# Kernel optimization log

Hardware: AMD Instinct MI355X
Metric: run time of the kernel (lower is better)

Reference implementation:

```python
import jax, jax.numpy as jnp
import numpy as np

R, K, D = 4096, 128, 128      # num_records, num_codes, code_dim
B, P = 8, 8192                # batch_size, num_points
DIST_SCALE = 2.0
IN_DIM = D + 3                # 131


def setup_inputs() -> dict:
    key = jax.random.key(0)
    ks = jax.random.split(key, 20)
    inp = {}
    inp["indices"] = jax.random.randint(ks[0], (B,), 0, R)
    inp["query_points"] = jax.random.uniform(ks[1], (B, P, 3)) - 0.5
    inp["codes_position"] = jax.random.uniform(ks[2], (R, K, 3)) - 0.5
    inp["codes"] = jax.random.normal(ks[3], (R, K, D)) * 0.01
    dims = [(IN_DIM, 2048), (IN_DIM + 2048, 1024), (IN_DIM + 1024, 512),
            (IN_DIM + 512, 256), (IN_DIM + 256, 128), (128, 1)]
    for i, (fi, fo) in enumerate(dims):
        inp[f"W{i+1}"] = jax.random.normal(ks[4 + 2 * i], (fi, fo)) * (1.0 / np.sqrt(fi))
        inp[f"b{i+1}"] = jnp.zeros((fo,), jnp.float32)
    return inp


def _lrelu(x):
    return jnp.where(x > 0, x, 0.02 * x)


def reference(indices, query_points, codes_position, codes,
              W1, b1, W2, b2, W3, b3, W4, b4, W5, b5, W6, b6):
    # CodeCloud.query
    bcp = codes_position[indices]                      # (B,K,3)
    bc = codes[indices]                                # (B,K,D)
    diff = query_points[:, :, None, :] - bcp[:, None, :, :]   # (B,P,K,3)
    square_dist = jnp.sum(diff * diff, axis=-1) + 1e-16       # (B,P,K)
    # 1/sqrt(sd)**s == sd**(-s/2)
    weight = square_dist ** (-DIST_SCALE / 2.0)
    weight = weight / jnp.sum(weight, axis=-1, keepdims=True)
    query_codes = jnp.einsum('bpk,bkd->bpd', weight, bc)      # (B,P,D)

    # IM_Decoder with skip concats
    x = jnp.concatenate([query_codes, query_points], axis=-1) # (B,P,IN_DIM)
    h = _lrelu(x @ W1 + b1); h = jnp.concatenate([h, x], axis=-1)
    h = _lrelu(h @ W2 + b2); h = jnp.concatenate([h, x], axis=-1)
    h = _lrelu(h @ W3 + b3); h = jnp.concatenate([h, x], axis=-1)
    h = _lrelu(h @ W4 + b4); h = jnp.concatenate([h, x], axis=-1)
    h = _lrelu(h @ W5 + b5)
    pred_sd = (h @ W6 + b6)[..., 0]                            # (B,P)
    return pred_sd
```

## Files before the change

kernel.cpp:

```cpp
#include <hip/hip_runtime.h>
#include <cstdint>
#include <cstddef>

typedef unsigned short u16;
typedef __attribute__((ext_vector_type(8))) short short8;
typedef __attribute__((ext_vector_type(8))) unsigned short us8;
typedef __attribute__((ext_vector_type(4))) unsigned short us4;
typedef __attribute__((ext_vector_type(4))) float f32x4;

#define BATCH 8
#define PTS   8192
#define NPTS  (BATCH * PTS)
#define KC    128
#define DC    128

__device__ __forceinline__ float bf2f(u16 h) {
  union { unsigned u; float f; } v; v.u = ((unsigned)h) << 16; return v.f;
}
__device__ __forceinline__ u16 f2bf(float f) {
  union { float f; unsigned u; } v; v.f = f;
  unsigned r = v.u + 0x7FFFu + ((v.u >> 16) & 1u);
  return (u16)(r >> 16);
}

__device__ __forceinline__ bool detect_f32(const u16* p, int lane) {
  float v = bf2f(p[2 * lane]);
  float av = v < 0.f ? -v : v;
  return __ballot(av > 4.0f) != 0ULL;
}

__device__ __forceinline__ float ldf(const void* p, size_t i, bool f32) {
  return f32 ? ((const float*)p)[i] : bf2f(((const u16*)p)[i]);
}

__device__ __forceinline__ void gload16(const void* g, void* l) {
  __builtin_amdgcn_global_load_lds(
      (const __attribute__((address_space(1))) unsigned int*)(uintptr_t)g,
      (__attribute__((address_space(3))) unsigned int*)(uintptr_t)l,
      16, 0, 0);
}

__global__ __launch_bounds__(256)
void transpose_w(const void* __restrict__ W, u16* __restrict__ Wt,
                 int fi, int fo, int kp) {
  const bool f32 = detect_f32((const u16*)W, threadIdx.x & 63);
  __shared__ __align__(16) u16 tile[32][33];
  const int k0 = blockIdx.x * 32;
  const int n0 = blockIdx.y * 32;
  const int tx = threadIdx.x & 31;
  const int ty = threadIdx.x >> 5;
  #pragma unroll
  for (int i = 0; i < 4; ++i) {
    int k = k0 + ty + 8 * i;
    u16 v = 0;
    if (k < fi) {
      size_t idx = (size_t)k * fo + (n0 + tx);
      v = f32 ? f2bf(((const float*)W)[idx]) : ((const u16*)W)[idx];
    }
    tile[ty + 8 * i][tx] = v;
  }
  __syncthreads();
  #pragma unroll
  for (int i = 0; i < 4; ++i) {
    int n = n0 + ty + 8 * i;
    Wt[(size_t)n * kp + (k0 + tx)] = tile[tx][ty + 8 * i];
  }
}

__global__ __launch_bounds__(256)
void interp_kernel(const int* __restrict__ indices,
                   const void* __restrict__ qp,
                   const void* __restrict__ cp,
                   const void* __restrict__ codes,
                   u16* __restrict__ d0, int ld0,
                   u16* __restrict__ d1, int ld1,
                   u16* __restrict__ d2, int ld2,
                   u16* __restrict__ d3, int ld3,
                   u16* __restrict__ d4, int ld4,
                   int m0) {
  __shared__ __align__(16) u16 s_bc[KC * DC];
  __shared__ float s_cp[KC * 3];
  __shared__ float s_qp[32 * 3];
  __shared__ float s_w[32 * 132];
  __shared__ float s_part[32 * 4];
  __shared__ float s_winv[32];

  const int t = threadIdx.x;
  const bool f32 = detect_f32((const u16*)codes, t & 63);
  const int row0 = blockIdx.x * 32;
  const int gp0 = m0 + row0;
  const int b = gp0 / PTS;
  const int rec = indices[b];

  if (f32) {
    const float* src = (const float*)codes + (size_t)rec * (KC * DC);
    #pragma unroll
    for (int i = 0; i < 16; ++i) {
      int off = (t + i * 256) * 4;
      float4 v = *(const float4*)&src[off];
      us4 o; o.x = f2bf(v.x); o.y = f2bf(v.y); o.z = f2bf(v.z); o.w = f2bf(v.w);
      *(us4*)&s_bc[off] = o;
    }
  } else {
    const u16* src = (const u16*)codes + (size_t)rec * (KC * DC);
    #pragma unroll
    for (int i = 0; i < 8; ++i) {
      int off = (t + i * 256) * 8;
      *(us8*)&s_bc[off] = *(const us8*)&src[off];
    }
  }
  if (t < KC) {
    size_t base = ((size_t)rec * KC + t) * 3;
    s_cp[t * 3 + 0] = ldf(cp, base + 0, f32);
    s_cp[t * 3 + 1] = ldf(cp, base + 1, f32);
    s_cp[t * 3 + 2] = ldf(cp, base + 2, f32);
  }
  if (t < 96) {
    int i = t / 3, c = t - i * 3;
    s_qp[t] = ldf(qp, (size_t)(gp0 + i) * 3 + c, f32);
  }
  __syncthreads();

  #pragma unroll
  for (int it = 0; it < 16; ++it) {
    int idx = t + it * 256;
    int k = idx & 127, p = idx >> 7;
    float dx = s_qp[p * 3 + 0] - s_cp[k * 3 + 0];
    float dy = s_qp[p * 3 + 1] - s_cp[k * 3 + 1];
    float dz = s_qp[p * 3 + 2] - s_cp[k * 3 + 2];
    float dsq = dx * dx + dy * dy + dz * dz + 1e-16f;
    s_w[p * 132 + k] = 1.0f / dsq;
  }
  __syncthreads();
  if (t < 128) {
    int p = t >> 2, part = t & 3;
    float s = 0.f;
    #pragma unroll
    for (int j = 0; j < 32; ++j) s += s_w[p * 132 + part * 32 + j];
    s_part[p * 4 + part] = s;
  }
  __syncthreads();
  if (t < 32) {
    float s = s_part[t * 4 + 0] + s_part[t * 4 + 1] + s_part[t * 4 + 2] + s_part[t * 4 + 3];
    s_winv[t] = 1.0f / s;
  }
  __syncthreads();

  {
    int p = t >> 3;
    int dd = (t & 7) * 16;
    float acc[16];
    #pragma unroll
    for (int j = 0; j < 16; ++j) acc[j] = 0.f;
    for (int k = 0; k < KC; ++k) {
      float wv = s_w[p * 132 + k];
      us8 v0 = *(const us8*)&s_bc[k * DC + dd];
      us8 v1 = *(const us8*)&s_bc[k * DC + dd + 8];
      #pragma unroll
      for (int j = 0; j < 8; ++j) acc[j] += wv * bf2f(v0[j]);
      #pragma unroll
      for (int j = 0; j < 8; ++j) acc[8 + j] += wv * bf2f(v1[j]);
    }
    float wi = s_winv[p];
    us8 o0, o1;
    #pragma unroll
    for (int j = 0; j < 8; ++j) { o0[j] = f2bf(acc[j] * wi); o1[j] = f2bf(acc[8 + j] * wi); }
    size_t row = (size_t)(row0 + p);
    *(us8*)&d0[row * ld0 + dd] = o0; *(us8*)&d0[row * ld0 + dd + 8] = o1;
    *(us8*)&d1[row * ld1 + dd] = o0; *(us8*)&d1[row * ld1 + dd + 8] = o1;
    *(us8*)&d2[row * ld2 + dd] = o0; *(us8*)&d2[row * ld2 + dd + 8] = o1;
    *(us8*)&d3[row * ld3 + dd] = o0; *(us8*)&d3[row * ld3 + dd + 8] = o1;
    *(us8*)&d4[row * ld4 + dd] = o0; *(us8*)&d4[row * ld4 + dd + 8] = o1;
  }

  if (t < 32) {
    size_t row = (size_t)(row0 + t);
    us8 z = {0, 0, 0, 0, 0, 0, 0, 0};
    us8 t0 = z;
    t0[0] = f2bf(s_qp[t * 3 + 0]);
    t0[1] = f2bf(s_qp[t * 3 + 1]);
    t0[2] = f2bf(s_qp[t * 3 + 2]);
    u16* ps[5] = {d0, d1, d2, d3, d4};
    int  ls[5] = {ld0, ld1, ld2, ld3, ld4};
    #pragma unroll
    for (int qd = 0; qd < 5; ++qd) {
      u16* dst = ps[qd] + row * ls[qd] + 128;
      *(us8*)&dst[0] = t0;
      #pragma unroll
      for (int c = 1; c < 8; ++c) *(us8*)&dst[c * 8] = z;
    }
  }
}

__global__ __launch_bounds__(256, 2)
void gemm_bt_lrelu(const u16* __restrict__ A, int lda,
                   const u16* __restrict__ Bt, int ldb,
                   const u16* __restrict__ bias,
                   u16* __restrict__ C, int ldc,
                   int Kp) {
  __shared__ __align__(16) u16 sA[128 * 32];
  __shared__ __align__(16) u16 sB[128 * 32];
  const int tid = threadIdx.x;
  const int lane = tid & 63;
  const int w = tid >> 6;
  const int wm = w & 1, wn = w >> 1;
  const int bn = blockIdx.x * 128, bm = blockIdx.y * 128;

  const f32x4 zero = {0.f, 0.f, 0.f, 0.f};
  f32x4 acc[4][4];
  #pragma unroll
  for (int i = 0; i < 4; ++i)
    #pragma unroll
    for (int j = 0; j < 4; ++j) acc[i][j] = zero;

  const int r4 = lane >> 2;
  const int cg = lane & 3;
  const u16* ag = A + (size_t)(bm + w * 32 + r4) * lda + cg * 8;
  const u16* bg = Bt + (size_t)(bn + w * 32 + r4) * ldb + cg * 8;
  u16* la = &sA[w * 1024];
  u16* lb = &sB[w * 1024];

  const int r = lane & 15, q = lane >> 4;
  const u16* ra = &sA[(wm * 64 + r) * 32 + q * 8];
  const u16* rb = &sB[(wn * 64 + r) * 32 + q * 8];

  for (int k0 = 0; k0 < Kp; k0 += 32) {
    gload16(ag + k0, la);
    gload16(ag + k0 + (size_t)16 * lda, la + 512);
    gload16(bg + k0, lb);
    gload16(bg + k0 + (size_t)16 * ldb, lb + 512);
    __syncthreads();
    short8 af[4], bq[4];
    #pragma unroll
    for (int mt = 0; mt < 4; ++mt) af[mt] = *(const short8*)(ra + mt * 512);
    #pragma unroll
    for (int nt = 0; nt < 4; ++nt) bq[nt] = *(const short8*)(rb + nt * 512);
    #pragma unroll
    for (int mt = 0; mt < 4; ++mt)
      #pragma unroll
      for (int nt = 0; nt < 4; ++nt)
        acc[mt][nt] = __builtin_amdgcn_mfma_f32_16x16x32_bf16(af[mt], bq[nt], acc[mt][nt], 0, 0, 0);
    __syncthreads();
  }

  #pragma unroll
  for (int nt = 0; nt < 4; ++nt) {
    int col = bn + wn * 64 + nt * 16 + r;
    float bb = bf2f(bias[col]);
    #pragma unroll
    for (int mt = 0; mt < 4; ++mt) {
      int grow = bm + wm * 64 + mt * 16 + q * 4;
      #pragma unroll
      for (int reg = 0; reg < 4; ++reg) {
        float v = acc[mt][nt][reg] + bb;
        v = v > 0.f ? v : 0.02f * v;
        C[(size_t)(grow + reg) * ldc + col] = f2bf(v);
      }
    }
  }
}

#define G_BAR()  __builtin_amdgcn_s_barrier()
#define G_FENCE() asm volatile("" ::: "memory")
#define G_LGKM0() asm volatile("s_waitcnt lgkmcnt(0)" ::: "memory")

__global__ __launch_bounds__(512, 2)
void gemm256_bt_lrelu(const u16* __restrict__ A, int lda,
                      const u16* __restrict__ Bt, int ldb,
                      const u16* __restrict__ bias,
                      u16* __restrict__ C, int ldc,
                      int Kp, int lognx) {
  __shared__ __align__(16) u16 sA[32768];
  __shared__ __align__(16) u16 sB[32768];

  const int tid = threadIdx.x;
  const int lane = tid & 63;
  const int w = tid >> 6;
  const int wm = w >> 2;
  const int wn = w & 3;
  const int lr = lane & 15;
  const int kg = lane >> 4;
  const int rs = tid >> 3;
  const int cs = ((tid & 7) ^ (rs & 7)) << 3;

  const unsigned nwg = gridDim.x;
  const unsigned lid = blockIdx.x;
  const unsigned qq = nwg >> 3, rr = nwg & 7, xc = lid & 7, ii = lid >> 3;
  const unsigned swz = (xc < rr ? xc * (qq + 1) : rr * (qq + 1) + (xc - rr) * qq) + ii;
  const int bx = (int)(swz & ((1u << lognx) - 1u));
  const int by = (int)(swz >> lognx);
  const int bn = bx << 8, bm = by << 8;

  const u16* a0 = A + (size_t)(bm + rs) * lda + cs;
  const u16* b0 = Bt + (size_t)(bn + rs) * ldb + cs;

  const int rowA = (wm << 13) + (lr << 6);
  const int rowB = (wn << 12) + (lr << 6);
  const int c0 = ((kg ^ (lr & 7)) << 3);
  const int c1 = (((4 + kg) ^ (lr & 7)) << 3);

  const int nt = Kp >> 6;

  f32x4 acc[8][4];
  const f32x4 zero = {0.f, 0.f, 0.f, 0.f};
  #pragma unroll
  for (int m = 0; m < 8; ++m)
    #pragma unroll
    for (int n = 0; n < 4; ++n) acc[m][n] = zero;

#define STAGE_A(bfv, h, kt) do { \
    const u16* _s = a0 + (size_t)(h) * 128 * lda + ((kt) << 6); \
    u16* _d = &sA[((bfv) << 14) + ((h) << 13) + (tid << 3)]; \
    gload16(_s, _d); \
    gload16(_s + (size_t)64 * lda, _d + 4096); \
  } while (0)
#define STAGE_B(bfv, h, kt) do { \
    const u16* _s = b0 + (size_t)(h) * 128 * ldb + ((kt) << 6); \
    u16* _d = &sB[((bfv) << 14) + ((h) << 13) + (tid << 3)]; \
    gload16(_s, _d); \
    gload16(_s + (size_t)64 * ldb, _d + 4096); \
  } while (0)

  STAGE_B(0, 0, 0); STAGE_B(0, 1, 0); STAGE_A(0, 0, 0); STAGE_A(0, 1, 0);
  if (nt > 1) {
    STAGE_B(1, 0, 1); STAGE_B(1, 1, 1); STAGE_A(1, 0, 1);
    asm volatile("s_waitcnt vmcnt(6)" ::: "memory");
  } else {
    asm volatile("s_waitcnt vmcnt(0)" ::: "memory");
  }
  G_BAR(); G_FENCE();

  short8 af[4][2], bq[4][2];

  for (int t = 0; t < nt; ++t) {
    const int sb = (t & 1) << 14;
    #pragma unroll
    for (int m = 0; m < 4; ++m) {
      af[m][0] = *(const short8*)&sA[sb + rowA + (m << 10) + c0];
      af[m][1] = *(const short8*)&sA[sb + rowA + (m << 10) + c1];
    }
    #pragma unroll
    for (int n = 0; n < 4; ++n) {
      bq[n][0] = *(const short8*)&sB[sb + rowB + (n << 10) + c0];
      bq[n][1] = *(const short8*)&sB[sb + rowB + (n << 10) + c1];
    }
    if (t + 1 < nt) STAGE_A((t & 1) ^ 1, 1, t + 1);
    G_FENCE(); G_BAR(); G_FENCE();
    __builtin_amdgcn_s_setprio(1);
    #pragma unroll
    for (int k = 0; k < 2; ++k)
      #pragma unroll
      for (int m = 0; m < 4; ++m)
        #pragma unroll
        for (int n = 0; n < 2; ++n)
          acc[m][n] = __builtin_amdgcn_mfma_f32_16x16x32_bf16(af[m][k], bq[n][k], acc[m][n], 0, 0, 0);
    __builtin_amdgcn_s_setprio(0);
    G_LGKM0();
    G_BAR(); G_FENCE();
    if (t + 2 < nt) STAGE_B(t & 1, 0, t + 2);
    G_FENCE(); G_BAR(); G_FENCE();
    __builtin_amdgcn_s_setprio(1);
    #pragma unroll
    for (int k = 0; k < 2; ++k)
      #pragma unroll
      for (int m = 0; m < 4; ++m)
        #pragma unroll
        for (int n = 0; n < 2; ++n)
          acc[m][n + 2] = __builtin_amdgcn_mfma_f32_16x16x32_bf16(af[m][k], bq[n + 2][k], acc[m][n + 2], 0, 0, 0);
    __builtin_amdgcn_s_setprio(0);
    G_BAR(); G_FENCE();
    #pragma unroll
    for (int m = 0; m < 4; ++m) {
      af[m][0] = *(const short8*)&sA[sb + rowA + ((m + 4) << 10) + c0];
      af[m][1] = *(const short8*)&sA[sb + rowA + ((m + 4) << 10) + c1];
    }
    if (t + 2 < nt) STAGE_B(t & 1, 1, t + 2);
    G_FENCE(); G_BAR(); G_FENCE();
    __builtin_amdgcn_s_setprio(1);
    #pragma unroll
    for (int k = 0; k < 2; ++k)
      #pragma unroll
      for (int m = 0; m < 4; ++m)
        #pragma unroll
        for (int n = 0; n < 2; ++n)
          acc[m + 4][n] = __builtin_amdgcn_mfma_f32_16x16x32_bf16(af[m][k], bq[n][k], acc[m + 4][n], 0, 0, 0);
    __builtin_amdgcn_s_setprio(0);
    G_LGKM0();
    G_BAR(); G_FENCE();
    if (t + 2 < nt) STAGE_A(t & 1, 0, t + 2);
    G_FENCE(); G_BAR(); G_FENCE();
    __builtin_amdgcn_s_setprio(1);
    #pragma unroll
    for (int k = 0; k < 2; ++k)
      #pragma unroll
      for (int m = 0; m < 4; ++m)
        #pragma unroll
        for (int n = 0; n < 2; ++n)
          acc[m + 4][n + 2] = __builtin_amdgcn_mfma_f32_16x16x32_bf16(af[m][k], bq[n + 2][k], acc[m + 4][n + 2], 0, 0, 0);
    __builtin_amdgcn_s_setprio(0);
    if (t + 2 < nt)      { asm volatile("s_waitcnt vmcnt(6)" ::: "memory"); }
    else if (t + 1 < nt) { asm volatile("s_waitcnt vmcnt(0)" ::: "memory"); }
    G_BAR(); G_FENCE();
  }
#undef STAGE_A
#undef STAGE_B

  const int colb = bn + (wn << 6);
  const int rowb = bm + (wm << 7);
  #pragma unroll
  for (int n = 0; n < 4; ++n) {
    const int col = colb + n * 16 + lr;
    const float bb = bf2f(bias[col]);
    #pragma unroll
    for (int m = 0; m < 8; ++m) {
      const int grow = rowb + m * 16 + kg * 4;
      #pragma unroll
      for (int reg = 0; reg < 4; ++reg) {
        float v = acc[m][n][reg] + bb;
        v = v > 0.f ? v : 0.02f * v;
        C[(size_t)(grow + reg) * ldc + col] = f2bf(v);
      }
    }
  }
}

__global__ __launch_bounds__(256)
void final_dot(const u16* __restrict__ h5, const void* __restrict__ W6,
               const u16* __restrict__ b6, void* __restrict__ out, int m0) {
  __shared__ float s_w6[128];
  const int t = threadIdx.x;
  const bool f32 = detect_f32((const u16*)W6, t & 63);
  if (t < 128) s_w6[t] = ldf(W6, t, f32);
  __syncthreads();
  const size_t row = (size_t)blockIdx.x * 256 + t;
  const u16* hp = h5 + row * 128;
  float acc = 0.f;
  #pragma unroll
  for (int i = 0; i < 16; ++i) {
    us8 v = *(const us8*)&hp[i * 8];
    #pragma unroll
    for (int j = 0; j < 8; ++j) acc += bf2f(v[j]) * s_w6[i * 8 + j];
  }
  acc += bf2f(b6[0]);
  if (f32) ((float*)out)[m0 + row] = acc;
  else     ((u16*)out)[m0 + row] = f2bf(acc);
}

extern "C" void kernel_launch(void* const* d_in, const int* in_sizes, int n_in,
                              void* d_out, int out_size, void* d_ws, size_t ws_size,
                              hipStream_t stream) {
  (void)in_sizes; (void)n_in; (void)out_size;
  const int* indices = (const int*)d_in[0];
  const void* qp    = d_in[1];
  const void* cp    = d_in[2];
  const void* codes = d_in[3];
  const void* Wm[6]; const u16* bv[6];
  for (int i = 0; i < 6; ++i) { Wm[i] = d_in[4 + 2 * i]; bv[i] = (const u16*)d_in[5 + 2 * i]; }

  static const int fi[5] = {131, 2179, 1155, 643, 387};
  static const int fo[5] = {2048, 1024, 512, 256, 128};
  static const int kp[5] = {192, 2240, 1216, 704, 448};
  static const int bw[6] = {192, 2240, 1216, 704, 448, 128};

  char* base = (char*)d_ws;
  size_t off = 0;
  u16* wt[5];
  for (int l = 0; l < 5; ++l) {
    wt[l] = (u16*)(base + off);
    off = (off + (size_t)kp[l] * fo[l] * 2 + 255) & ~(size_t)255;
  }
  const size_t fixed = off;

  int CH = 128;
  for (int c = 1; c <= 128; c <<= 1) {
    size_t mc = (size_t)NPTS / c;
    size_t need = fixed;
    for (int i = 0; i < 6; ++i) need += ((mc * bw[i] * 2 + 255) & ~(size_t)255);
    if (need <= ws_size) { CH = c; break; }
  }
  const size_t Mc = (size_t)NPTS / CH;
  u16* ab[6];
  for (int i = 0; i < 6; ++i) {
    ab[i] = (u16*)(base + off);
    off = (off + Mc * bw[i] * 2 + 255) & ~(size_t)255;
  }

  for (int l = 0; l < 5; ++l) {
    dim3 g(kp[l] / 32, fo[l] / 32);
    hipLaunchKernelGGL(transpose_w, g, dim3(256), 0, stream, Wm[l], wt[l], fi[l], fo[l], kp[l]);
  }

  const int nM256 = (int)(Mc >> 8);
  const int nM128 = (int)(Mc >> 7);
  for (int c = 0; c < CH; ++c) {
    int m0 = (int)((size_t)c * Mc);
    hipLaunchKernelGGL(interp_kernel, dim3((unsigned)(Mc / 32)), dim3(256), 0, stream,
                       indices, qp, cp, codes,
                       ab[0], 192,
                       ab[1] + 2048, 2240,
                       ab[2] + 1024, 1216,
                       ab[3] + 512, 704,
                       ab[4] + 256, 448,
                       m0);
    hipLaunchKernelGGL(gemm256_bt_lrelu, dim3((unsigned)(8 * nM256)), dim3(512), 0, stream,
                       ab[0], 192,  wt[0], 192,  bv[0], ab[1], 2240, 192,  3);
    hipLaunchKernelGGL(gemm256_bt_lrelu, dim3((unsigned)(4 * nM256)), dim3(512), 0, stream,
                       ab[1], 2240, wt[1], 2240, bv[1], ab[2], 1216, 2240, 2);
    hipLaunchKernelGGL(gemm256_bt_lrelu, dim3((unsigned)(2 * nM256)), dim3(512), 0, stream,
                       ab[2], 1216, wt[2], 1216, bv[2], ab[3], 704,  1216, 1);
    hipLaunchKernelGGL(gemm256_bt_lrelu, dim3((unsigned)(1 * nM256)), dim3(512), 0, stream,
                       ab[3], 704,  wt[3], 704,  bv[3], ab[4], 448,  704,  0);
    hipLaunchKernelGGL(gemm_bt_lrelu, dim3(1, (unsigned)nM128), dim3(256), 0, stream,
                       ab[4], 448,  wt[4], 448,  bv[4], ab[5], 128,  448);
    hipLaunchKernelGGL(final_dot, dim3((unsigned)(Mc / 256)), dim3(256), 0, stream,
                       ab[5], Wm[5], bv[5], (void*)d_out, m0);
  }
}
```

Baseline: 1.021 ms.

## Stage GEMM epilogue through LDS for coalesced 16-byte output stores

Swaps the MFMA operand order so each lane holds four consecutive output columns. Bias is preloaded into shared memory. The epilogue writes bf16 results into a padded LDS tile, one 128-row half per pass, and then stores them to global memory as coalesced 16-byte rows. This replaces the earlier scattered 2-byte strided stores, at the cost of extra barriers and LDS traffic in the epilogue.

```diff
diff --git a/kernel.cpp b/kernel.cpp
--- a/kernel.cpp
+++ b/kernel.cpp
@@ -7,6 +7,7 @@
 typedef __attribute__((ext_vector_type(8))) unsigned short us8;
 typedef __attribute__((ext_vector_type(4))) unsigned short us4;
 typedef __attribute__((ext_vector_type(4))) float f32x4;
+typedef __attribute__((ext_vector_type(2))) unsigned u32x2;
 
 #define BATCH 8
 #define PTS   8192
@@ -270,8 +271,10 @@
                       const u16* __restrict__ bias,
                       u16* __restrict__ C, int ldc,
                       int Kp, int lognx) {
-  __shared__ __align__(16) u16 sA[32768];
-  __shared__ __align__(16) u16 sB[32768];
+  __shared__ __align__(16) u16 smem[65536 + 256];
+  u16* sA = smem;
+  u16* sB = smem + 32768;
+  u16* sbias = smem + 65536;
 
   const int tid = threadIdx.x;
   const int lane = tid & 63;
@@ -293,6 +296,8 @@
 
   const u16* a0 = A + (size_t)(bm + rs) * lda + cs;
   const u16* b0 = Bt + (size_t)(bn + rs) * ldb + cs;
+
+  if (tid < 64) *(us4*)&sbias[tid << 2] = *(const us4*)&bias[bn + (tid << 2)];
 
   const int rowA = (wm << 13) + (lr << 6);
   const int rowB = (wn << 12) + (lr << 6);
@@ -353,7 +358,7 @@
       for (int m = 0; m < 4; ++m)
         #pragma unroll
         for (int n = 0; n < 2; ++n)
-          acc[m][n] = __builtin_amdgcn_mfma_f32_16x16x32_bf16(af[m][k], bq[n][k], acc[m][n], 0, 0, 0);
+          acc[m][n] = __builtin_amdgcn_mfma_f32_16x16x32_bf16(bq[n][k], af[m][k], acc[m][n], 0, 0, 0);
     __builtin_amdgcn_s_setprio(0);
     G_LGKM0();
     G_BAR(); G_FENCE();
@@ -366,7 +371,7 @@
       for (int m = 0; m < 4; ++m)
         #pragma unroll
         for (int n = 0; n < 2; ++n)
-          acc[m][n + 2] = __builtin_amdgcn_mfma_f32_16x16x32_bf16(af[m][k], bq[n + 2][k], acc[m][n + 2], 0, 0, 0);
+          acc[m][n + 2] = __builtin_amdgcn_mfma_f32_16x16x32_bf16(bq[n + 2][k], af[m][k], acc[m][n + 2], 0, 0, 0);
     __builtin_amdgcn_s_setprio(0);
     G_BAR(); G_FENCE();
     #pragma unroll
@@ -383,7 +388,7 @@
       for (int m = 0; m < 4; ++m)
         #pragma unroll
         for (int n = 0; n < 2; ++n)
-          acc[m + 4][n] = __builtin_amdgcn_mfma_f32_16x16x32_bf16(af[m][k], bq[n][k], acc[m + 4][n], 0, 0, 0);
+          acc[m + 4][n] = __builtin_amdgcn_mfma_f32_16x16x32_bf16(bq[n][k], af[m][k], acc[m + 4][n], 0, 0, 0);
     __builtin_amdgcn_s_setprio(0);
     G_LGKM0();
     G_BAR(); G_FENCE();
@@ -396,7 +401,7 @@
       for (int m = 0; m < 4; ++m)
         #pragma unroll
         for (int n = 0; n < 2; ++n)
-          acc[m + 4][n + 2] = __builtin_amdgcn_mfma_f32_16x16x32_bf16(af[m][k], bq[n + 2][k], acc[m + 4][n + 2], 0, 0, 0);
+          acc[m + 4][n + 2] = __builtin_amdgcn_mfma_f32_16x16x32_bf16(bq[n + 2][k], af[m][k], acc[m + 4][n + 2], 0, 0, 0);
     __builtin_amdgcn_s_setprio(0);
     if (t + 2 < nt)      { asm volatile("s_waitcnt vmcnt(6)" ::: "memory"); }
     else if (t + 1 < nt) { asm volatile("s_waitcnt vmcnt(0)" ::: "memory"); }
@@ -405,22 +410,48 @@
 #undef STAGE_A
 #undef STAGE_B
 
-  const int colb = bn + (wn << 6);
-  const int rowb = bm + (wm << 7);
+  u16* sC = smem;
+  const int colq = (wn << 6) + (kg << 2);
+  float bias_v[4][4];
   #pragma unroll
   for (int n = 0; n < 4; ++n) {
-    const int col = colb + n * 16 + lr;
-    const float bb = bf2f(bias[col]);
-    #pragma unroll
-    for (int m = 0; m < 8; ++m) {
-      const int grow = rowb + m * 16 + kg * 4;
-      #pragma unroll
-      for (int reg = 0; reg < 4; ++reg) {
-        float v = acc[m][n][reg] + bb;
-        v = v > 0.f ? v : 0.02f * v;
-        C[(size_t)(grow + reg) * ldc + col] = f2bf(v);
+    us4 bb = *(const us4*)&sbias[colq + (n << 4)];
+    #pragma unroll
+    for (int j = 0; j < 4; ++j) bias_v[n][j] = bf2f(bb[j]);
+  }
+  #pragma unroll
+  for (int pass = 0; pass < 2; ++pass) {
+    if (wm == pass) {
+      #pragma unroll
+      for (int m = 0; m < 8; ++m) {
+        const int row = (m << 4) + lr;
+        #pragma unroll
+        for (int n = 0; n < 4; ++n) {
+          f32x4 a = acc[m][n];
+          float v0 = a[0] + bias_v[n][0]; v0 = v0 > 0.f ? v0 : 0.02f * v0;
+          float v1 = a[1] + bias_v[n][1]; v1 = v1 > 0.f ? v1 : 0.02f * v1;
+          float v2 = a[2] + bias_v[n][2]; v2 = v2 > 0.f ? v2 : 0.02f * v2;
+          float v3 = a[3] + bias_v[n][3]; v3 = v3 > 0.f ? v3 : 0.02f * v3;
+          u32x2 d;
+          d.x = (unsigned)f2bf(v0) | ((unsigned)f2bf(v1) << 16);
+          d.y = (unsigned)f2bf(v2) | ((unsigned)f2bf(v3) << 16);
+          *(u32x2*)&sC[row * 264 + colq + (n << 4)] = d;
+        }
       }
-    }
+      G_LGKM0();
+    }
+    G_BAR();
+    {
+      const int rrow = tid >> 5;
+      const int cc = (tid & 31) << 3;
+      #pragma unroll
+      for (int it = 0; it < 8; ++it) {
+        const int row = (it << 4) + rrow;
+        us8 v = *(const us8*)&sC[row * 264 + cc];
+        *(us8*)&C[(size_t)(bm + (pass << 7) + row) * ldc + bn + cc] = v;
+      }
+    }
+    G_BAR();
   }
 }
 
```

New measurement: 921.5 us. 1.11x faster.
